# Kernel optimization log

Hardware: AMD Instinct MI355X
Metric: run time of the kernel (lower is better)

## Reference

```python
import jax, jax.numpy as jnp
import numpy as np

BN_EPS = 1e-5

def _bn_train(h, gamma, beta):
    # BatchNorm1d in training mode: batch statistics over the node dim
    mean = jnp.mean(h, axis=0)
    var = jnp.mean((h - mean) ** 2, axis=0)  # biased variance, as torch BN uses for normalization
    return gamma * (h - mean) * jax.lax.rsqrt(var + BN_EPS) + beta


def setup_inputs() -> dict:
    key = jax.random.key(0)
    ks = jax.random.split(key, 8)
    N, E = 100000, 1250000
    d_in, d_out = 64, 128
    x = jax.random.normal(ks[0], (N, d_in), dtype=jnp.float32)
    edge_index = jax.random.randint(ks[1], (2, E), 0, N, dtype=jnp.int64)
    s1 = 1.0 / np.sqrt(d_in)
    s2 = 1.0 / np.sqrt(d_out)
    W1 = jax.random.uniform(ks[2], (d_in, d_out), dtype=jnp.float32, minval=-s1, maxval=s1)
    b1 = jax.random.uniform(ks[3], (d_out,), dtype=jnp.float32, minval=-s1, maxval=s1)
    g1 = jnp.ones((d_out,), dtype=jnp.float32)
    be1 = jnp.zeros((d_out,), dtype=jnp.float32)
    W2 = jax.random.uniform(ks[4], (d_out, d_out), dtype=jnp.float32, minval=-s2, maxval=s2)
    b2 = jax.random.uniform(ks[5], (d_out,), dtype=jnp.float32, minval=-s2, maxval=s2)
    g2 = jnp.ones((d_out,), dtype=jnp.float32)
    be2 = jnp.zeros((d_out,), dtype=jnp.float32)
    return {"x": x, "edge_index": edge_index, "W1": W1, "b1": b1, "g1": g1, "be1": be1,
            "W2": W2, "b2": b2, "g2": g2, "be2": be2}


def reference(x, edge_index, W1, b1, g1, be1, W2, b2, g2, be2):
    src = edge_index[0]
    dst = edge_index[1]
    N = x.shape[0]
    # GIN aggregation: sum of neighbor features scattered to destination nodes
    agg = jax.ops.segment_sum(x[src], dst, num_segments=N)
    h = x + agg  # (1 + eps) * x + agg with eps = 0 (GINConv default)
    # MLP: Linear -> ReLU -> BN -> Linear -> ReLU -> BN
    h = jnp.maximum(h @ W1 + b1, 0.0)
    h = _bn_train(h, g1, be1)
    h = jnp.maximum(h @ W2 + b2, 0.0)
    h = _bn_train(h, g2, be2)
    return h
```

## Files before the change

kernel.cpp:

```cpp
#include <hip/hip_runtime.h>


typedef unsigned short u16;
typedef unsigned int   u32;
typedef __attribute__((ext_vector_type(8))) short  s8v;
typedef __attribute__((ext_vector_type(4))) float  f4v;

#define NBMAX 512
#define CAP   8192
#define CPB   4096

__device__ __forceinline__ u16 f2bf(float f) {
    u32 u = __builtin_bit_cast(u32, f);
    return (u16)((u + 0x7FFFu + ((u >> 16) & 1u)) >> 16);
}
__device__ __forceinline__ float bf2f(u16 h) {
    u32 u = ((u32)h) << 16;
    return __builtin_bit_cast(float, u);
}
__device__ __forceinline__ uint4 pk8(const u16* p) {
    uint4 r;
    r.x = (u32)p[0] | ((u32)p[1] << 16);
    r.y = (u32)p[2] | ((u32)p[3] << 16);
    r.z = (u32)p[4] | ((u32)p[5] << 16);
    r.w = (u32)p[6] | ((u32)p[7] << 16);
    return r;
}

__global__ __launch_bounds__(512) void k_zero(int* __restrict__ gcnt,
                                              float* __restrict__ stats)
{
    int t = threadIdx.x;
    gcnt[t] = 0;
    stats[t] = 0.f;
}

__global__ __launch_bounds__(256) void k_part(const int* __restrict__ ei, int E,
                                              int* __restrict__ gcnt,
                                              unsigned int* __restrict__ pk)
{
    __shared__ int cnt[NBMAX];
    __shared__ int gbase[NBMAX];
    const int tid = threadIdx.x;
    const int e0 = blockIdx.x * CPB;
    const int e1 = min(E, e0 + CPB);

    for (int i = tid; i < NBMAX; i += 256) cnt[i] = 0;
    __syncthreads();

    for (int e = e0 + tid; e < e1; e += 256)
        atomicAdd(&cnt[ei[E + e] >> 8], 1);
    __syncthreads();

    for (int i = tid; i < NBMAX; i += 256)
        gbase[i] = cnt[i] ? atomicAdd(&gcnt[i], cnt[i]) : 0;
    __syncthreads();
    for (int i = tid; i < NBMAX; i += 256) cnt[i] = 0;
    __syncthreads();

    for (int e = e0 + tid; e < e1; e += 256) {
        int dst = ei[E + e];
        int src = ei[e];
        int b = dst >> 8;
        int lr = atomicAdd(&cnt[b], 1);
        pk[(long)b * CAP + gbase[b] + lr] =
            ((unsigned)(dst & 255) << 17) | (unsigned)src;
    }
}

__global__ __launch_bounds__(256) void k_csr(const unsigned int* __restrict__ pk,
                                             const int* __restrict__ gcnt,
                                             int* __restrict__ nbr,
                                             int* __restrict__ beg,
                                             int* __restrict__ endq, int N)
{
    __shared__ int lcnt[256];
    __shared__ int lscan[256];
    const int tid = threadIdx.x;
    const int b = blockIdx.x;
    const int cnt = gcnt[b];
    const unsigned int* eb = pk + (long)b * CAP;

    lcnt[tid] = 0;
    __syncthreads();
    for (int j = tid; j < cnt; j += 256)
        atomicAdd(&lcnt[eb[j] >> 17], 1);
    __syncthreads();

    int v = lcnt[tid];
    lscan[tid] = v;
    __syncthreads();
    for (int off = 1; off < 256; off <<= 1) {
        int t = (tid >= off) ? lscan[tid - off] : 0;
        __syncthreads();
        lscan[tid] += t;
        __syncthreads();
    }
    int excl = lscan[tid] - v;

    int node = (b << 8) + tid;
    if (node < N) {
        beg[node]  = b * CAP + excl;
        endq[node] = b * CAP + excl + v;
    }
    lcnt[tid] = excl;
    __syncthreads();

    for (int j = tid; j < cnt; j += 256) {
        unsigned int p = eb[j];
        int lr = atomicAdd(&lcnt[p >> 17], 1);
        nbr[b * CAP + lr] = (int)(p & 0x1FFFFu);
    }
}

__global__ __launch_bounds__(256) void k_gather(const float4* __restrict__ x4,
                                                const int* __restrict__ beg,
                                                const int* __restrict__ endq,
                                                const int* __restrict__ nbr,
                                                float4* __restrict__ h04, int N)
{
    int wid  = threadIdx.x >> 6;
    int lane = threadIdx.x & 63;
    int node = blockIdx.x * 4 + wid;
    if (node >= N) return;
    int d4 = lane & 15;
    int g  = lane >> 4;
    int b = beg[node], e = endq[node];

    float4 acc = make_float4(0.f, 0.f, 0.f, 0.f);
    if (g == 0) acc = x4[(long)node * 16 + d4];

    for (int j = b + g; j < e; j += 4) {
        int s = nbr[j];
        float4 v = x4[(long)s * 16 + d4];
        acc.x += v.x; acc.y += v.y; acc.z += v.z; acc.w += v.w;
    }

#pragma unroll
    for (int m = 16; m <= 32; m <<= 1) {
        acc.x += __shfl_xor(acc.x, m, 64);
        acc.y += __shfl_xor(acc.y, m, 64);
        acc.z += __shfl_xor(acc.z, m, 64);
        acc.w += __shfl_xor(acc.w, m, 64);
    }

    if (g == 0) h04[(long)node * 16 + d4] = acc;
}

__global__ void k_wprep(const float* __restrict__ W1,
                        u16* __restrict__ w1th, u16* __restrict__ w1tl)
{
    int j = threadIdx.x;
    for (int k = 0; k < 64; ++k) {
        float w = W1[k * 128 + j];
        u16 h = f2bf(w);
        w1th[j * 64 + k] = h;
        w1tl[j * 64 + k] = f2bf(w - bf2f(h));
    }
}

template<int K>
__global__ __launch_bounds__(256) void k_gemm_mfma(
    const float* __restrict__ A, const u16* __restrict__ WTh,
    const u16* __restrict__ WTl, const float* __restrict__ bias,
    float* __restrict__ Out, int N,
    float* __restrict__ sums, float* __restrict__ sqs)
{
    __shared__ u16 sAh[128][40], sAl[128][40];
    __shared__ u16 sBh[128][40], sBl[128][40];
    __shared__ float lsum[128], lsq[128];

    const int tid  = threadIdx.x;
    const int lane = tid & 63, wid = tid >> 6;
    const int wr = wid >> 1, wc = wid & 1;
    const int cq = lane & 15, rq = lane >> 4;
    const int koff = rq * 8;
    const int row0 = blockIdx.x * 128;
    const int sr = tid >> 1;
    const int hf = tid & 1;

    if (tid < 128) { lsum[tid] = 0.f; lsq[tid] = 0.f; }

    f4v acc[4][4];
#pragma unroll
    for (int i = 0; i < 4; ++i)
#pragma unroll
        for (int j = 0; j < 4; ++j)
#pragma unroll
            for (int e = 0; e < 4; ++e) acc[i][j][e] = 0.f;

    for (int k0 = 0; k0 < K; k0 += 32) {
        __syncthreads();
        {
            float v[16];
            int grow = row0 + sr;
            if (grow < N) {
                const float4* src = (const float4*)(A + (long)grow * K + k0 + hf * 16);
#pragma unroll
                for (int i = 0; i < 4; ++i) {
                    float4 f = src[i];
                    v[4*i] = f.x; v[4*i+1] = f.y; v[4*i+2] = f.z; v[4*i+3] = f.w;
                }
            } else {
#pragma unroll
                for (int i = 0; i < 16; ++i) v[i] = 0.f;
            }
            u16 hh[16], ll[16];
#pragma unroll
            for (int i = 0; i < 16; ++i) {
                hh[i] = f2bf(v[i]);
                ll[i] = f2bf(v[i] - bf2f(hh[i]));
            }
            *(uint4*)&sAh[sr][hf*16]     = pk8(hh);
            *(uint4*)&sAh[sr][hf*16 + 8] = pk8(hh + 8);
            *(uint4*)&sAl[sr][hf*16]     = pk8(ll);
            *(uint4*)&sAl[sr][hf*16 + 8] = pk8(ll + 8);
        }
        {
            const uint4* sh = (const uint4*)(WTh + (long)sr * K + k0 + hf * 16);
            const uint4* sl = (const uint4*)(WTl + (long)sr * K + k0 + hf * 16);
            *(uint4*)&sBh[sr][hf*16]     = sh[0];
            *(uint4*)&sBh[sr][hf*16 + 8] = sh[1];
            *(uint4*)&sBl[sr][hf*16]     = sl[0];
            *(uint4*)&sBl[sr][hf*16 + 8] = sl[1];
        }
        __syncthreads();

        s8v ah[4], al[4];
#pragma unroll
        for (int tr = 0; tr < 4; ++tr) {
            int rr = wr * 64 + tr * 16 + cq;
            ah[tr] = __builtin_bit_cast(s8v, *(const uint4*)&sAh[rr][koff]);
            al[tr] = __builtin_bit_cast(s8v, *(const uint4*)&sAl[rr][koff]);
        }
#pragma unroll
        for (int tc = 0; tc < 4; ++tc) {
            int cc = wc * 64 + tc * 16 + cq;
            s8v bh = __builtin_bit_cast(s8v, *(const uint4*)&sBh[cc][koff]);
            s8v bl = __builtin_bit_cast(s8v, *(const uint4*)&sBl[cc][koff]);
#pragma unroll
            for (int tr = 0; tr < 4; ++tr) {
                acc[tr][tc] = __builtin_amdgcn_mfma_f32_16x16x32_bf16(ah[tr], bh, acc[tr][tc], 0, 0, 0);
                acc[tr][tc] = __builtin_amdgcn_mfma_f32_16x16x32_bf16(al[tr], bh, acc[tr][tc], 0, 0, 0);
                acc[tr][tc] = __builtin_amdgcn_mfma_f32_16x16x32_bf16(ah[tr], bl, acc[tr][tc], 0, 0, 0);
            }
        }
    }

#pragma unroll
    for (int tc = 0; tc < 4; ++tc) {
        int col = wc * 64 + tc * 16 + cq;
        float b = bias[col];
        float s = 0.f, q = 0.f;
#pragma unroll
        for (int tr = 0; tr < 4; ++tr) {
#pragma unroll
            for (int e = 0; e < 4; ++e) {
                int row = row0 + wr * 64 + tr * 16 + rq * 4 + e;
                if (row < N) {
                    float o = fmaxf(acc[tr][tc][e] + b, 0.f);
                    Out[(long)row * 128 + col] = o;
                    s += o;
                    q = fmaf(o, o, q);
                }
            }
        }
        s += __shfl_xor(s, 16, 64); s += __shfl_xor(s, 32, 64);
        q += __shfl_xor(q, 16, 64); q += __shfl_xor(q, 32, 64);
        if (lane < 16) {
            atomicAdd(&lsum[col], s);
            atomicAdd(&lsq[col],  q);
        }
    }
    __syncthreads();
    if (tid < 128) {
        atomicAdd(&sums[tid], lsum[tid]);
        atomicAdd(&sqs[tid],  lsq[tid]);
    }
}

__global__ void k_bn_fold(const float* __restrict__ stats,
                          const float* __restrict__ gamma, const float* __restrict__ beta,
                          const float* __restrict__ W2, const float* __restrict__ b2,
                          u16* __restrict__ w2th, u16* __restrict__ w2tl,
                          float* __restrict__ b2p, float invN)
{
    __shared__ float as[128], cs[128];
    int j = threadIdx.x;
    float m = stats[j] * invN;
    float v = stats[128 + j] * invN - m * m;
    float a = gamma[j] * rsqrtf(v + 1e-5f);
    float c = beta[j] - m * a;
    as[j] = a;
    cs[j] = c;
    __syncthreads();
    float bb = b2[j];
    for (int k = 0; k < 128; ++k) {
        float w  = W2[k * 128 + j];
        float wp = as[k] * w;
        u16 h = f2bf(wp);
        w2th[j * 128 + k] = h;
        w2tl[j * 128 + k] = f2bf(wp - bf2f(h));
        bb = fmaf(cs[k], w, bb);
    }
    b2p[j] = bb;
}

__global__ void k_bn_coeffs(const float* __restrict__ stats,
                            const float* __restrict__ gamma, const float* __restrict__ beta,
                            float* __restrict__ ac, float invN)
{
    int j = threadIdx.x;
    float m = stats[j] * invN;
    float v = stats[128 + j] * invN - m * m;
    float a = gamma[j] * rsqrtf(v + 1e-5f);
    ac[j] = a;
    ac[128 + j] = beta[j] - m * a;
}

__global__ __launch_bounds__(256) void k_bn_apply(float* __restrict__ out,
                                                  const float* __restrict__ ac, long n4)
{
    __shared__ float sa[128], sc[128];
    if (threadIdx.x < 128) {
        sa[threadIdx.x] = ac[threadIdx.x];
        sc[threadIdx.x] = ac[128 + threadIdx.x];
    }
    __syncthreads();
    long i = (long)blockIdx.x * 256 + threadIdx.x;
    if (i < n4) {
        float4 v = ((float4*)out)[i];
        int c0 = (int)((i * 4) & 127);
        v.x = fmaf(v.x, sa[c0 + 0], sc[c0 + 0]);
        v.y = fmaf(v.y, sa[c0 + 1], sc[c0 + 1]);
        v.z = fmaf(v.z, sa[c0 + 2], sc[c0 + 2]);
        v.w = fmaf(v.w, sa[c0 + 3], sc[c0 + 3]);
        ((float4*)out)[i] = v;
    }
}

extern "C" void kernel_launch(void* const* d_in, const int* in_sizes, int n_in,
                              void* d_out, int out_size, void* d_ws, size_t ws_size,
                              hipStream_t stream)
{
    const float* x   = (const float*)d_in[0];
    const int*   ei  = (const int*)  d_in[1];
    const float* W1  = (const float*)d_in[2];
    const float* b1  = (const float*)d_in[3];
    const float* g1  = (const float*)d_in[4];
    const float* be1 = (const float*)d_in[5];
    const float* W2  = (const float*)d_in[6];
    const float* b2  = (const float*)d_in[7];
    const float* g2  = (const float*)d_in[8];
    const float* be2 = (const float*)d_in[9];
    float* out = (float*)d_out;

    const int N = in_sizes[0] / 64;
    const int E = in_sizes[1] / 2;
    const int nbuckets = (N + 255) >> 8;

    float* ws    = (float*)d_ws;
    float* h0    = ws;
    float* h1    = h0 + (long)N * 64;
    float* b2p   = h1 + (long)N * 128;
    float* stats = b2p + 128;
    float* ac    = stats + 512;
    int*   gcnt  = (int*)(ac + 256);
    u16*   w1th  = (u16*)(gcnt + NBMAX);
    u16*   w1tl  = w1th + 128 * 64;
    u16*   w2th  = w1tl + 128 * 64;
    u16*   w2tl  = w2th + 128 * 128;

    unsigned int* pk   = (unsigned int*)h1;
    int*          nbr  = (int*)h1 + (long)NBMAX * CAP;
    int*          beg  = nbr + (long)NBMAX * CAP;
    int*          endq = beg + N;

    const float invN = 1.0f / (float)N;

    k_zero<<<1, 512, 0, stream>>>(gcnt, stats);

    k_wprep<<<1, 128, 0, stream>>>(W1, w1th, w1tl);

    k_part<<<(E + CPB - 1) / CPB, 256, 0, stream>>>(ei, E, gcnt, pk);

    k_csr<<<nbuckets, 256, 0, stream>>>(pk, gcnt, nbr, beg, endq, N);

    k_gather<<<(N + 3) / 4, 256, 0, stream>>>((const float4*)x, beg, endq, nbr,
                                              (float4*)h0, N);

    int gB = (N + 127) / 128;
    k_gemm_mfma<64><<<gB, 256, 0, stream>>>(h0, w1th, w1tl, b1, h1, N,
                                            stats, stats + 128);

    k_bn_fold<<<1, 128, 0, stream>>>(stats, g1, be1, W2, b2, w2th, w2tl,
                                     b2p, invN);

    k_gemm_mfma<128><<<gB, 256, 0, stream>>>(h1, w2th, w2tl, b2p, out, N,
                                             stats + 256, stats + 384);

    k_bn_coeffs<<<1, 128, 0, stream>>>(stats + 256, g2, be2, ac, invN);

    long n4o = (long)N * 128 / 4;
    k_bn_apply<<<(int)((n4o + 255) / 256), 256, 0, stream>>>(out, ac, n4o);
}
```

Baseline: 321.4 us.

## Pre-split activations into packed bf16 hi/lo pairs and restructure GEMM staging

The gather and first GEMM epilogue now write activations as packed bf16 hi/lo pairs in 32-bit words, so the GEMMs no longer perform the float-to-split conversion in their load loops. The GEMM stages 64-wide K chunks into wider shared tiles and prefetches the second chunk into registers, cutting K-loop iterations and barriers. The single-thread-block BN fold is replaced by a coefficient kernel plus a 128-block parallel weight fold with a tree reduction. It adds one launch and more registers and LDS per block, which may lower occupancy.

```diff
diff --git a/kernel.cpp b/kernel.cpp
--- a/kernel.cpp
+++ b/kernel.cpp
@@ -18,13 +18,10 @@
     u32 u = ((u32)h) << 16;
     return __builtin_bit_cast(float, u);
 }
-__device__ __forceinline__ uint4 pk8(const u16* p) {
-    uint4 r;
-    r.x = (u32)p[0] | ((u32)p[1] << 16);
-    r.y = (u32)p[2] | ((u32)p[3] << 16);
-    r.z = (u32)p[4] | ((u32)p[5] << 16);
-    r.w = (u32)p[6] | ((u32)p[7] << 16);
-    return r;
+__device__ __forceinline__ u32 packsplit(float f) {
+    u16 h = f2bf(f);
+    u16 l = f2bf(f - bf2f(h));
+    return ((u32)h << 16) | (u32)l;
 }
 
 __global__ __launch_bounds__(512) void k_zero(int* __restrict__ gcnt,
@@ -117,7 +114,7 @@
                                                 const int* __restrict__ beg,
                                                 const int* __restrict__ endq,
                                                 const int* __restrict__ nbr,
-                                                float4* __restrict__ h04, int N)
+                                                uint4* __restrict__ h0pk, int N)
 {
     int wid  = threadIdx.x >> 6;
     int lane = threadIdx.x & 63;
@@ -144,7 +141,14 @@
         acc.w += __shfl_xor(acc.w, m, 64);
     }
 
-    if (g == 0) h04[(long)node * 16 + d4] = acc;
+    if (g == 0) {
+        uint4 p;
+        p.x = packsplit(acc.x);
+        p.y = packsplit(acc.y);
+        p.z = packsplit(acc.z);
+        p.w = packsplit(acc.w);
+        h0pk[(long)node * 16 + d4] = p;
+    }
 }
 
 __global__ void k_wprep(const float* __restrict__ W1,
@@ -159,22 +163,21 @@
     }
 }
 
-template<int K>
+template<int K, int PACK>
 __global__ __launch_bounds__(256) void k_gemm_mfma(
-    const float* __restrict__ A, const u16* __restrict__ WTh,
+    const u32* __restrict__ Apk, const u16* __restrict__ WTh,
     const u16* __restrict__ WTl, const float* __restrict__ bias,
-    float* __restrict__ Out, int N,
+    u32* __restrict__ OutP, float* __restrict__ OutF, int N,
     float* __restrict__ sums, float* __restrict__ sqs)
 {
-    __shared__ u16 sAh[128][40], sAl[128][40];
-    __shared__ u16 sBh[128][40], sBl[128][40];
+    __shared__ u16 sAh[128][72], sAl[128][72];
+    __shared__ u16 sBh[128][72], sBl[128][72];
     __shared__ float lsum[128], lsq[128];
 
     const int tid  = threadIdx.x;
     const int lane = tid & 63, wid = tid >> 6;
     const int wr = wid >> 1, wc = wid & 1;
     const int cq = lane & 15, rq = lane >> 4;
-    const int koff = rq * 8;
     const int row0 = blockIdx.x * 128;
     const int sr = tid >> 1;
     const int hf = tid & 1;
@@ -189,60 +192,104 @@
 #pragma unroll
             for (int e = 0; e < 4; ++e) acc[i][j][e] = 0.f;
 
-    for (int k0 = 0; k0 < K; k0 += 32) {
-        __syncthreads();
-        {
-            float v[16];
-            int grow = row0 + sr;
-            if (grow < N) {
-                const float4* src = (const float4*)(A + (long)grow * K + k0 + hf * 16);
-#pragma unroll
-                for (int i = 0; i < 4; ++i) {
-                    float4 f = src[i];
-                    v[4*i] = f.x; v[4*i+1] = f.y; v[4*i+2] = f.z; v[4*i+3] = f.w;
+    uint4 ar[8], brh[4], brl[4];
+
+    {
+        int grow = row0 + sr;
+        if (grow < N) {
+            const uint4* ap = (const uint4*)(Apk + (long)grow * K + hf * 32);
+#pragma unroll
+            for (int i = 0; i < 8; ++i) ar[i] = ap[i];
+        } else {
+#pragma unroll
+            for (int i = 0; i < 8; ++i) ar[i] = make_uint4(0, 0, 0, 0);
+        }
+        const uint4* bh = (const uint4*)(WTh + (long)sr * K + hf * 32);
+        const uint4* bl = (const uint4*)(WTl + (long)sr * K + hf * 32);
+#pragma unroll
+        for (int i = 0; i < 4; ++i) { brh[i] = bh[i]; brl[i] = bl[i]; }
+    }
+#pragma unroll
+    for (int i = 0; i < 8; ++i) {
+        int e0 = hf * 32 + i * 4;
+        u32 u[4] = {ar[i].x, ar[i].y, ar[i].z, ar[i].w};
+        u16 hh[4], ll[4];
+#pragma unroll
+        for (int t = 0; t < 4; ++t) { hh[t] = (u16)(u[t] >> 16); ll[t] = (u16)(u[t] & 0xFFFFu); }
+        *(uint2*)&sAh[sr][e0] = make_uint2((u32)hh[0] | ((u32)hh[1] << 16),
+                                           (u32)hh[2] | ((u32)hh[3] << 16));
+        *(uint2*)&sAl[sr][e0] = make_uint2((u32)ll[0] | ((u32)ll[1] << 16),
+                                           (u32)ll[2] | ((u32)ll[3] << 16));
+    }
+#pragma unroll
+    for (int i = 0; i < 4; ++i) {
+        int e0 = hf * 32 + i * 8;
+        *(uint4*)&sBh[sr][e0] = brh[i];
+        *(uint4*)&sBl[sr][e0] = brl[i];
+    }
+    __syncthreads();
+
+    if (K == 128) {
+        int grow = row0 + sr;
+        if (grow < N) {
+            const uint4* ap = (const uint4*)(Apk + (long)grow * K + 64 + hf * 32);
+#pragma unroll
+            for (int i = 0; i < 8; ++i) ar[i] = ap[i];
+        } else {
+#pragma unroll
+            for (int i = 0; i < 8; ++i) ar[i] = make_uint4(0, 0, 0, 0);
+        }
+        const uint4* bh = (const uint4*)(WTh + (long)sr * K + 64 + hf * 32);
+        const uint4* bl = (const uint4*)(WTl + (long)sr * K + 64 + hf * 32);
+#pragma unroll
+        for (int i = 0; i < 4; ++i) { brh[i] = bh[i]; brl[i] = bl[i]; }
+    }
+
+    const int NSTEP = K / 64;
+    for (int s = 0; s < NSTEP; ++s) {
+        if (s == 1) {
+            __syncthreads();
+#pragma unroll
+            for (int i = 0; i < 8; ++i) {
+                int e0 = hf * 32 + i * 4;
+                u32 u[4] = {ar[i].x, ar[i].y, ar[i].z, ar[i].w};
+                u16 hh[4], ll[4];
+#pragma unroll
+                for (int t = 0; t < 4; ++t) { hh[t] = (u16)(u[t] >> 16); ll[t] = (u16)(u[t] & 0xFFFFu); }
+                *(uint2*)&sAh[sr][e0] = make_uint2((u32)hh[0] | ((u32)hh[1] << 16),
+                                                   (u32)hh[2] | ((u32)hh[3] << 16));
+                *(uint2*)&sAl[sr][e0] = make_uint2((u32)ll[0] | ((u32)ll[1] << 16),
+                                                   (u32)ll[2] | ((u32)ll[3] << 16));
+            }
+#pragma unroll
+            for (int i = 0; i < 4; ++i) {
+                int e0 = hf * 32 + i * 8;
+                *(uint4*)&sBh[sr][e0] = brh[i];
+                *(uint4*)&sBl[sr][e0] = brl[i];
+            }
+            __syncthreads();
+        }
+#pragma unroll
+        for (int kk = 0; kk < 2; ++kk) {
+            const int koff = kk * 32 + rq * 8;
+            s8v ah[4], al[4];
+#pragma unroll
+            for (int tr = 0; tr < 4; ++tr) {
+                int rr = wr * 64 + tr * 16 + cq;
+                ah[tr] = __builtin_bit_cast(s8v, *(const uint4*)&sAh[rr][koff]);
+                al[tr] = __builtin_bit_cast(s8v, *(const uint4*)&sAl[rr][koff]);
+            }
+#pragma unroll
+            for (int tc = 0; tc < 4; ++tc) {
+                int cc = wc * 64 + tc * 16 + cq;
+                s8v bh = __builtin_bit_cast(s8v, *(const uint4*)&sBh[cc][koff]);
+                s8v bl = __builtin_bit_cast(s8v, *(const uint4*)&sBl[cc][koff]);
+#pragma unroll
+                for (int tr = 0; tr < 4; ++tr) {
+                    acc[tr][tc] = __builtin_amdgcn_mfma_f32_16x16x32_bf16(ah[tr], bh, acc[tr][tc], 0, 0, 0);
+                    acc[tr][tc] = __builtin_amdgcn_mfma_f32_16x16x32_bf16(al[tr], bh, acc[tr][tc], 0, 0, 0);
+                    acc[tr][tc] = __builtin_amdgcn_mfma_f32_16x16x32_bf16(ah[tr], bl, acc[tr][tc], 0, 0, 0);
                 }
-            } else {
-#pragma unroll
-                for (int i = 0; i < 16; ++i) v[i] = 0.f;
-            }
-            u16 hh[16], ll[16];
-#pragma unroll
-            for (int i = 0; i < 16; ++i) {
-                hh[i] = f2bf(v[i]);
-                ll[i] = f2bf(v[i] - bf2f(hh[i]));
-            }
-            *(uint4*)&sAh[sr][hf*16]     = pk8(hh);
-            *(uint4*)&sAh[sr][hf*16 + 8] = pk8(hh + 8);
-            *(uint4*)&sAl[sr][hf*16]     = pk8(ll);
-            *(uint4*)&sAl[sr][hf*16 + 8] = pk8(ll + 8);
-        }
-        {
-            const uint4* sh = (const uint4*)(WTh + (long)sr * K + k0 + hf * 16);
-            const uint4* sl = (const uint4*)(WTl + (long)sr * K + k0 + hf * 16);
-            *(uint4*)&sBh[sr][hf*16]     = sh[0];
-            *(uint4*)&sBh[sr][hf*16 + 8] = sh[1];
-            *(uint4*)&sBl[sr][hf*16]     = sl[0];
-            *(uint4*)&sBl[sr][hf*16 + 8] = sl[1];
-        }
-        __syncthreads();
-
-        s8v ah[4], al[4];
-#pragma unroll
-        for (int tr = 0; tr < 4; ++tr) {
-            int rr = wr * 64 + tr * 16 + cq;
-            ah[tr] = __builtin_bit_cast(s8v, *(const uint4*)&sAh[rr][koff]);
-            al[tr] = __builtin_bit_cast(s8v, *(const uint4*)&sAl[rr][koff]);
-        }
-#pragma unroll
-        for (int tc = 0; tc < 4; ++tc) {
-            int cc = wc * 64 + tc * 16 + cq;
-            s8v bh = __builtin_bit_cast(s8v, *(const uint4*)&sBh[cc][koff]);
-            s8v bl = __builtin_bit_cast(s8v, *(const uint4*)&sBl[cc][koff]);
-#pragma unroll
-            for (int tr = 0; tr < 4; ++tr) {
-                acc[tr][tc] = __builtin_amdgcn_mfma_f32_16x16x32_bf16(ah[tr], bh, acc[tr][tc], 0, 0, 0);
-                acc[tr][tc] = __builtin_amdgcn_mfma_f32_16x16x32_bf16(al[tr], bh, acc[tr][tc], 0, 0, 0);
-                acc[tr][tc] = __builtin_amdgcn_mfma_f32_16x16x32_bf16(ah[tr], bl, acc[tr][tc], 0, 0, 0);
             }
         }
     }
@@ -259,7 +306,8 @@
                 int row = row0 + wr * 64 + tr * 16 + rq * 4 + e;
                 if (row < N) {
                     float o = fmaxf(acc[tr][tc][e] + b, 0.f);
-                    Out[(long)row * 128 + col] = o;
+                    if (PACK) OutP[(long)row * 128 + col] = packsplit(o);
+                    else      OutF[(long)row * 128 + col] = o;
                     s += o;
                     q = fmaf(o, o, q);
                 }
@@ -277,33 +325,6 @@
         atomicAdd(&sums[tid], lsum[tid]);
         atomicAdd(&sqs[tid],  lsq[tid]);
     }
-}
-
-__global__ void k_bn_fold(const float* __restrict__ stats,
-                          const float* __restrict__ gamma, const float* __restrict__ beta,
-                          const float* __restrict__ W2, const float* __restrict__ b2,
-                          u16* __restrict__ w2th, u16* __restrict__ w2tl,
-                          float* __restrict__ b2p, float invN)
-{
-    __shared__ float as[128], cs[128];
-    int j = threadIdx.x;
-    float m = stats[j] * invN;
-    float v = stats[128 + j] * invN - m * m;
-    float a = gamma[j] * rsqrtf(v + 1e-5f);
-    float c = beta[j] - m * a;
-    as[j] = a;
-    cs[j] = c;
-    __syncthreads();
-    float bb = b2[j];
-    for (int k = 0; k < 128; ++k) {
-        float w  = W2[k * 128 + j];
-        float wp = as[k] * w;
-        u16 h = f2bf(wp);
-        w2th[j * 128 + k] = h;
-        w2tl[j * 128 + k] = f2bf(wp - bf2f(h));
-        bb = fmaf(cs[k], w, bb);
-    }
-    b2p[j] = bb;
 }
 
 __global__ void k_bn_coeffs(const float* __restrict__ stats,
@@ -316,6 +337,31 @@
     float a = gamma[j] * rsqrtf(v + 1e-5f);
     ac[j] = a;
     ac[128 + j] = beta[j] - m * a;
+}
+
+__global__ __launch_bounds__(128) void k_wfold(const float* __restrict__ ac1,
+                                               const float* __restrict__ W2,
+                                               const float* __restrict__ b2,
+                                               u16* __restrict__ w2th,
+                                               u16* __restrict__ w2tl,
+                                               float* __restrict__ b2p)
+{
+    __shared__ float red[128];
+    const int j = blockIdx.x;
+    const int k = threadIdx.x;
+    float w  = W2[k * 128 + j];
+    float wp = ac1[k] * w;
+    u16 h = f2bf(wp);
+    w2th[j * 128 + k] = h;
+    w2tl[j * 128 + k] = f2bf(wp - bf2f(h));
+    red[k] = ac1[128 + k] * w;
+    __syncthreads();
+#pragma unroll
+    for (int off = 64; off > 0; off >>= 1) {
+        if (k < off) red[k] += red[k + off];
+        __syncthreads();
+    }
+    if (k == 0) b2p[j] = b2[j] + red[0];
 }
 
 __global__ __launch_bounds__(256) void k_bn_apply(float* __restrict__ out,
@@ -360,19 +406,20 @@
     const int nbuckets = (N + 255) >> 8;
 
     float* ws    = (float*)d_ws;
-    float* h0    = ws;
-    float* h1    = h0 + (long)N * 64;
-    float* b2p   = h1 + (long)N * 128;
+    u32*   h0pk  = (u32*)ws;
+    u32*   h1pk  = h0pk + (long)N * 64;
+    float* b2p   = (float*)(h1pk + (long)N * 128);
     float* stats = b2p + 128;
-    float* ac    = stats + 512;
-    int*   gcnt  = (int*)(ac + 256);
+    float* ac1   = stats + 512;
+    float* ac2   = ac1 + 256;
+    int*   gcnt  = (int*)(ac2 + 256);
     u16*   w1th  = (u16*)(gcnt + NBMAX);
     u16*   w1tl  = w1th + 128 * 64;
     u16*   w2th  = w1tl + 128 * 64;
     u16*   w2tl  = w2th + 128 * 128;
 
-    unsigned int* pk   = (unsigned int*)h1;
-    int*          nbr  = (int*)h1 + (long)NBMAX * CAP;
+    unsigned int* pk   = (unsigned int*)h1pk;
+    int*          nbr  = (int*)h1pk + (long)NBMAX * CAP;
     int*          beg  = nbr + (long)NBMAX * CAP;
     int*          endq = beg + N;
 
@@ -387,20 +434,23 @@
     k_csr<<<nbuckets, 256, 0, stream>>>(pk, gcnt, nbr, beg, endq, N);
 
     k_gather<<<(N + 3) / 4, 256, 0, stream>>>((const float4*)x, beg, endq, nbr,
-                                              (float4*)h0, N);
+                                              (uint4*)h0pk, N);
 
     int gB = (N + 127) / 128;
-    k_gemm_mfma<64><<<gB, 256, 0, stream>>>(h0, w1th, w1tl, b1, h1, N,
-                                            stats, stats + 128);
-
-    k_bn_fold<<<1, 128, 0, stream>>>(stats, g1, be1, W2, b2, w2th, w2tl,
-                                     b2p, invN);
-
-    k_gemm_mfma<128><<<gB, 256, 0, stream>>>(h1, w2th, w2tl, b2p, out, N,
-                                             stats + 256, stats + 384);
-
-    k_bn_coeffs<<<1, 128, 0, stream>>>(stats + 256, g2, be2, ac, invN);
+    k_gemm_mfma<64, 1><<<gB, 256, 0, stream>>>(h0pk, w1th, w1tl, b1,
+                                               h1pk, nullptr, N,
+                                               stats, stats + 128);
+
+    k_bn_coeffs<<<1, 128, 0, stream>>>(stats, g1, be1, ac1, invN);
+
+    k_wfold<<<128, 128, 0, stream>>>(ac1, W2, b2, w2th, w2tl, b2p);
+
+    k_gemm_mfma<128, 0><<<gB, 256, 0, stream>>>(h1pk, w2th, w2tl, b2p,
+                                                nullptr, out, N,
+                                                stats + 256, stats + 384);
+
+    k_bn_coeffs<<<1, 128, 0, stream>>>(stats + 256, g2, be2, ac2, invN);
 
     long n4o = (long)N * 128 / 4;
-    k_bn_apply<<<(int)((n4o + 255) / 256), 256, 0, stream>>>(out, ac, n4o);
-}
+    k_bn_apply<<<(int)((n4o + 255) / 256), 256, 0, stream>>>(out, ac2, n4o);
+}
```

After: 309.8 us. -3.6%, faster.
